# Kernel tuning notes

Hardware: AMD Instinct MI355X
Metric: run time of the kernel (lower is better)

The kernel has to match this reference:

```python
import jax, jax.numpy as jnp
import numpy as np
from jax import lax

LRELU_SLOPE = 0.2
EPS = 1e-8


def eq_linear(x, W, b):
    # EqualizedLinear: weight scaled by 1/sqrt(fan_in)
    c = 1.0 / np.sqrt(W.shape[1])
    return x @ (W * c).T + b


def mod_conv(x, s, W, demod):
    # x: [b, cin, h, w], s: [b, cin], W: [cout, cin, k, k]
    b, cin, h, w = x.shape
    cout, _, k, _ = W.shape
    c = 1.0 / np.sqrt(cin * k * k)
    weights = (W * c)[None] * s[:, None, :, None, None]  # [b, cout, cin, k, k]
    if demod:
        sigma_inv = lax.rsqrt(jnp.sum(weights ** 2, axis=(2, 3, 4)) + EPS)  # [b, cout]
        weights = weights * sigma_inv[:, :, None, None, None]
    x2 = x.reshape(1, b * cin, h, w)
    wk = weights.reshape(b * cout, cin, k, k)
    pad = k // 2
    out = lax.conv_general_dilated(
        x2, wk, window_strides=(1, 1), padding=[(pad, pad), (pad, pad)],
        dimension_numbers=("NCHW", "OIHW", "NCHW"), feature_group_count=b)
    return out.reshape(b, cout, h, w)


def style_block(x, w, noise, style_W, style_b, conv_W, scale_noise, bias):
    A = eq_linear(w, style_W, style_b)          # [b, cin]
    x = mod_conv(x, A, conv_W, demod=True)      # [b, cout, h, w]
    if noise is not None:
        x = x + scale_noise[None, :, None, None] * noise
    return jax.nn.leaky_relu(x + bias[None, :, None, None], LRELU_SLOPE)


def rgb_block(x, w, style_W, style_b, conv_W, bias):
    A = eq_linear(w, style_W, style_b)
    x = mod_conv(x, A, conv_W, demod=False)     # 1x1 conv to 3 channels
    return jax.nn.leaky_relu(x + bias[None, :, None, None], LRELU_SLOPE)


def setup_inputs() -> dict:
    key = jax.random.key(0)
    ks = jax.random.split(key, 10)
    B, CIN, COUT, WD, H, W = 8, 512, 512, 512, 64, 64
    return {
        "x": jax.random.normal(ks[0], (B, CIN, H, W), jnp.float32),
        "w": jax.random.normal(ks[1], (B, WD), jnp.float32),
        "noise": jax.random.normal(ks[2], (2, B, 1, H, W), jnp.float32),
        # StyleBlock 1
        "s1_style_W": jax.random.normal(ks[3], (CIN, WD), jnp.float32),
        "s1_style_b": jnp.ones((CIN,), jnp.float32),
        "s1_conv_W": jax.random.normal(ks[4], (COUT, CIN, 3, 3), jnp.float32),
        "s1_scale_noise": jnp.zeros((1,), jnp.float32),
        "s1_bias": jnp.zeros((COUT,), jnp.float32),
        # StyleBlock 2
        "s2_style_W": jax.random.normal(ks[5], (COUT, WD), jnp.float32),
        "s2_style_b": jnp.ones((COUT,), jnp.float32),
        "s2_conv_W": jax.random.normal(ks[6], (COUT, COUT, 3, 3), jnp.float32),
        "s2_scale_noise": jnp.zeros((1,), jnp.float32),
        "s2_bias": jnp.zeros((COUT,), jnp.float32),
        # RGBBlock
        "rgb_style_W": jax.random.normal(ks[7], (COUT, WD), jnp.float32),
        "rgb_style_b": jnp.ones((COUT,), jnp.float32),
        "rgb_conv_W": jax.random.normal(ks[8], (3, COUT, 1, 1), jnp.float32),
        "rgb_bias": jnp.zeros((3,), jnp.float32),
    }


def reference(x, w, noise,
              s1_style_W, s1_style_b, s1_conv_W, s1_scale_noise, s1_bias,
              s2_style_W, s2_style_b, s2_conv_W, s2_scale_noise, s2_bias,
              rgb_style_W, rgb_style_b, rgb_conv_W, rgb_bias):
    x = style_block(x, w, noise[0], s1_style_W, s1_style_b, s1_conv_W, s1_scale_noise, s1_bias)
    x = style_block(x, w, noise[1], s2_style_W, s2_style_b, s2_conv_W, s2_scale_noise, s2_bias)
    rgb = rgb_block(x, w, rgb_style_W, rgb_style_b, rgb_conv_W, rgb_bias)
    return (x, rgb)
```

## Files before the change

kernel.cpp:

```cpp
#include <hip/hip_runtime.h>
#include <stdint.h>

typedef __attribute__((ext_vector_type(8))) short bf16x8;
typedef __attribute__((ext_vector_type(4))) float f32x4;

__device__ __forceinline__ ushort f2bf(float f) {
  uint32_t u = __builtin_bit_cast(uint32_t, f);
  u += 0x7fffu + ((u >> 16) & 1u);
  return (ushort)(u >> 16);
}

__device__ __forceinline__ void async_copy16(const void* gsrc, void* ldst) {
  __builtin_amdgcn_global_load_lds(
      (const __attribute__((address_space(1))) void*)gsrc,
      (__attribute__((address_space(3))) void*)ldst, 16, 0, 0);
}

__global__ void style_linear3(const float* __restrict__ w,
                              const float* __restrict__ sW1, const float* __restrict__ sb1,
                              const float* __restrict__ sW2, const float* __restrict__ sb2,
                              const float* __restrict__ sW3, const float* __restrict__ sb3,
                              float* __restrict__ A1, float* __restrict__ A2,
                              float* __restrict__ A3) {
  const int which = blockIdx.z;
  const float* sW = (which == 0) ? sW1 : (which == 1) ? sW2 : sW3;
  const float* sb = (which == 0) ? sb1 : (which == 1) ? sb2 : sb3;
  float* A = (which == 0) ? A1 : (which == 1) ? A2 : A3;
  const int b = blockIdx.y;
  const int lane = threadIdx.x & 63, wv = threadIdx.x >> 6;
  const int co = blockIdx.x * 4 + wv;
  const float c = 0.04419417382415922f;
  const float* wr = w + b * 512;
  const float* Wr = sW + (size_t)co * 512;
  float s = 0.f;
#pragma unroll
  for (int i = 0; i < 8; ++i) {
    const int d = i * 64 + lane;
    s += wr[d] * Wr[d];
  }
#pragma unroll
  for (int off = 32; off; off >>= 1) s += __shfl_xor(s, off);
  if (lane == 0) A[b * 512 + co] = s * c + sb[co];
}

__global__ void prep_sigma(const float* __restrict__ Wc, const float* __restrict__ A,
                           ushort* __restrict__ Wt, float* __restrict__ sig) {
  const int co = blockIdx.x;
  const int ci = threadIdx.x;
  const int lane = ci & 63, wid = ci >> 6;
  const float c = 0.014731391274719738f;
  const float* src = Wc + ((size_t)co * 512 + ci) * 9;
  float s = 0.f;
#pragma unroll
  for (int t = 0; t < 9; ++t) {
    float v = src[t] * c;
    Wt[(size_t)t * 262144 + co * 512 + ci] = f2bf(v);
    s += v * v;
  }
  __shared__ float red[8][8];
#pragma unroll
  for (int b = 0; b < 8; ++b) {
    float a = A[b * 512 + ci];
    float v = s * a * a;
#pragma unroll
    for (int off = 32; off; off >>= 1) v += __shfl_xor(v, off);
    if (lane == 0) red[b][wid] = v;
  }
  __syncthreads();
  if (ci < 8) {
    float t = 0.f;
#pragma unroll
    for (int wv = 0; wv < 8; ++wv) t += red[ci][wv];
    sig[ci * 512 + co] = rsqrtf(t + 1e-8f);
  }
}

__global__ void zero_border(uint4* __restrict__ x1, uint4* __restrict__ x2,
                            uint4* __restrict__ rgb) {
  const int i = blockIdx.x * 256 + threadIdx.x;
  const int per = 16640;
  const int tot = per * 8;
  if (i >= 2 * tot) {
    const int j = i - 2 * tot;
    if (j < 24576) rgb[j] = make_uint4(0u, 0u, 0u, 0u);
    return;
  }
  uint4* base = (i < tot) ? x1 : x2;
  int t = (i < tot) ? i : i - tot;
  const int bb = t / per;
  int r = t - bb * per;
  int row, cell, q;
  if (r < 8448) {
    row = (r >= 4224) ? 65 : 0;
    int pos = (r >= 4224) ? r - 4224 : r;
    cell = pos >> 6;
    q = pos & 63;
  } else {
    int r2 = r - 8448;
    row = 1 + (r2 >> 7);
    cell = ((r2 >> 6) & 1) ? 65 : 0;
    q = r2 & 63;
  }
  base[(((size_t)bb * 66 + row) * 66 + cell) * 64 + q] = make_uint4(0u, 0u, 0u, 0u);
}

__global__ void mod_transpose(const float* __restrict__ X, const float* __restrict__ A,
                              ushort* __restrict__ xs) {
  __shared__ float tile[128][65];
  const int h = blockIdx.x;
  const int ci0 = blockIdx.y * 128;
  const int b = blockIdx.z;
  const int tid = threadIdx.x;
  const int wcol = tid & 63;
  const int r0 = tid >> 6;
#pragma unroll 4
  for (int i = 0; i < 32; ++i) {
    const int cil = r0 + i * 4;
    const int ci = ci0 + cil;
    const size_t off = ((size_t)(b * 512 + ci) * 64 + h) * 64 + wcol;
    tile[cil][wcol] = X[off] * A[b * 512 + ci];
  }
  __syncthreads();
  const int sub = tid & 3;
  const int w = tid >> 2;
  ushort* dst = xs + (((size_t)b * 66 + (h + 1)) * 66 + (w + 1)) * 512 + ci0 + sub * 32;
#pragma unroll
  for (int g = 0; g < 4; ++g) {
    bf16x8 v;
#pragma unroll
    for (int j = 0; j < 8; ++j) v[j] = (short)f2bf(tile[sub * 32 + g * 8 + j][w]);
    *(bf16x8*)(dst + g * 8) = v;
  }
}

#define WAITVM(N) __builtin_amdgcn_s_waitcnt(0x0F70 | (N))
#define SGB __builtin_amdgcn_sched_group_barrier

#define READS(S, AF, BV)                                                     \
  do {                                                                       \
    const int q_ = (S) & 3;                                                  \
    const char* baA = (const char*)(&smA[0][0] + q_ * 8192);                 \
    const char* baB = (const char*)(&smB[0][0] + q_ * 8192);                 \
    _Pragma("unroll") for (int m_ = 0; m_ < 8; ++m_)                         \
        AF[m_] = *(const bf16x8*)(baA + aro[m_]);                            \
    _Pragma("unroll") for (int n_ = 0; n_ < 4; ++n_)                         \
        BV[n_] = *(const bf16x8*)(baB + bro[n_]);                            \
  } while (0)

#define PH(S, WN, DOREAD, DOSTAGE, RAF, RBV, MAF, MBV)                               \
  do {                                                                               \
    WAITVM(WN);                                                                      \
    __builtin_amdgcn_s_barrier();                                                    \
    __builtin_amdgcn_sched_barrier(0);                                               \
    __builtin_amdgcn_s_setprio(1);                                                   \
    if (DOREAD) READS((S) + 1, RAF, RBV);                                            \
    if (DOSTAGE) stage((S) + 3);                                                     \
    _Pragma("unroll") for (int m_ = 0; m_ < 8; ++m_)                                 \
      _Pragma("unroll") for (int n_ = 0; n_ < 4; ++n_)                               \
        acc[m_][n_] = __builtin_amdgcn_mfma_f32_16x16x32_bf16(MAF[m_], MBV[n_],      \
                                                              acc[m_][n_], 0, 0, 0); \
    SGB(0x8, 2, 0);                                                                  \
    SGB(0x100, 2, 0); SGB(0x8, 4, 0);                                                \
    SGB(0x100, 2, 0); SGB(0x8, 4, 0);                                                \
    SGB(0x100, 2, 0); SGB(0x8, 4, 0);                                                \
    SGB(0x100, 2, 0); SGB(0x8, 4, 0);                                                \
    SGB(0x100, 2, 0); SGB(0x8, 4, 0);                                                \
    SGB(0x100, 2, 0); SGB(0x8, 6, 0);                                                \
    __builtin_amdgcn_s_setprio(0);                                                   \
    __builtin_amdgcn_sched_barrier(0);                                               \
  } while (0)

template <int OUT_MODE>
__global__ __launch_bounds__(512, 2) void conv3x3(
    const ushort* __restrict__ xs, const ushort* __restrict__ Wt,
    const float* __restrict__ sig, const float* __restrict__ noise,
    const float* __restrict__ scale_noise, const float* __restrict__ bias,
    const float* __restrict__ amod, void* __restrict__ outp,
    const float* __restrict__ rgbw, const float* __restrict__ arr,
    float* __restrict__ outrgb) {
  __shared__ __align__(16) ushort smA[4][8192];
  __shared__ __align__(16) ushort smB[4][8192];
  const int tid = threadIdx.x, lane = tid & 63, wid = tid >> 6;
  const int wr = wid >> 2, wc = wid & 3;
  const int id = blockIdx.x;
  const int b = id & 7;
  const int tile = id >> 3;
  const int co0 = (tile & 1) * 256;
  const int px0 = (tile >> 1) * 256;
  const int h0 = px0 >> 6;

  const int sswz = ((lane & 3) ^ ((lane >> 3) & 3)) * 8;
  int aoff[2], boff[2];
  ushort *ldsA[2], *ldsB[2];
#pragma unroll
  for (int i = 0; i < 2; ++i) {
    const int row = (i * 8 + wid) * 16 + (lane >> 2);
    aoff[i] = (co0 + row) * 512 + sswz;
    const int hh = h0 + (row >> 6), ww = row & 63;
    boff[i] = ((b * 66 + hh) * 66 + ww) * 512 + sswz;
    ldsA[i] = &smA[0][0] + (i * 8 + wid) * 512 + lane * 8;
    ldsB[i] = &smB[0][0] + (i * 8 + wid) * 512 + lane * 8;
  }
  const int rdsw = ((lane >> 4) ^ ((lane >> 1) & 3)) * 16;
  int aro[8], bro[4];
#pragma unroll
  for (int m = 0; m < 8; ++m) aro[m] = (wr * 128 + m * 16 + (lane & 15)) * 64 + rdsw;
#pragma unroll
  for (int n = 0; n < 4; ++n) bro[n] = (wc * 64 + n * 16 + (lane & 15)) * 64 + rdsw;

  f32x4 acc[8][4];
#pragma unroll
  for (int m = 0; m < 8; ++m)
#pragma unroll
    for (int n = 0; n < 4; ++n) acc[m][n] = (f32x4){0.f, 0.f, 0.f, 0.f};

  auto stage = [&](int s) {
    const int tap = s >> 4;
    const int ci0 = (s & 15) << 5;
    const int kh = tap / 3;
    const int kw = tap - kh * 3;
    const int q = s & 3;
    const ushort* Wb = Wt + tap * 262144 + ci0;
    const ushort* Xb = xs + (kh * 66 + kw) * 512 + ci0;
    async_copy16(Wb + aoff[0], ldsA[0] + q * 8192);
    async_copy16(Wb + aoff[1], ldsA[1] + q * 8192);
    async_copy16(Xb + boff[0], ldsB[0] + q * 8192);
    async_copy16(Xb + boff[1], ldsB[1] + q * 8192);
  };

  bf16x8 afA[8], bvA[4], afB[8], bvB[4];

  stage(0);
  stage(1);
  stage(2);
  WAITVM(8);
  __builtin_amdgcn_s_barrier();
  __builtin_amdgcn_sched_barrier(0);
  READS(0, afA, bvA);

  for (int s = 0; s < 140; s += 2) {
    PH(s, 4, true, true, afB, bvB, afA, bvA);
    PH(s + 1, 4, true, true, afA, bvA, afB, bvB);
  }
  PH(140, 4, true, true, afB, bvB, afA, bvA);
  PH(141, 4, true, false, afA, bvA, afB, bvB);
  PH(142, 0, true, false, afB, bvB, afA, bvA);
  PH(143, 0, false, false, afA, bvA, afB, bvB);

  const float sn = scale_noise[0];
  const int colp = lane & 15;
  const int rq = (lane >> 4) * 4;
  float nz[4];
#pragma unroll
  for (int n = 0; n < 4; ++n)
    nz[n] = sn * noise[b * 4096 + px0 + wc * 64 + n * 16 + colp];
  float rgbp[3][4];
#pragma unroll
  for (int c = 0; c < 3; ++c)
#pragma unroll
    for (int n = 0; n < 4; ++n) rgbp[c][n] = 0.f;
#pragma unroll
  for (int m = 0; m < 8; ++m) {
    const int cob = co0 + wr * 128 + m * 16 + rq;
    float sg[4], bs[4], am[4];
    float w0[4], w1[4], w2[4];
#pragma unroll
    for (int r = 0; r < 4; ++r) {
      sg[r] = sig[b * 512 + cob + r];
      bs[r] = bias[cob + r];
      if (OUT_MODE == 0) {
        am[r] = amod[b * 512 + cob + r];
      } else {
        const float a3 = arr[b * 512 + cob + r] * 0.04419417382415922f;
        w0[r] = rgbw[cob + r] * a3;
        w1[r] = rgbw[512 + cob + r] * a3;
        w2[r] = rgbw[1024 + cob + r] * a3;
      }
    }
#pragma unroll
    for (int n = 0; n < 4; ++n) {
      const int px = px0 + wc * 64 + n * 16 + colp;
      if (OUT_MODE == 0) {
        const int hh = px >> 6, ww = px & 63;
        ushort pk[4];
#pragma unroll
        for (int r = 0; r < 4; ++r) {
          float v = acc[m][n][r] * sg[r] + nz[n] + bs[r];
          v = (v > 0.f) ? v : 0.2f * v;
          pk[r] = f2bf(v * am[r]);
        }
        uint2 u;
        u.x = (uint32_t)pk[0] | ((uint32_t)pk[1] << 16);
        u.y = (uint32_t)pk[2] | ((uint32_t)pk[3] << 16);
        *(uint2*)((ushort*)outp + (((size_t)b * 66 + hh + 1) * 66 + (ww + 1)) * 512 + cob) = u;
      } else {
#pragma unroll
        for (int r = 0; r < 4; ++r) {
          float v = acc[m][n][r] * sg[r] + nz[n] + bs[r];
          v = (v > 0.f) ? v : 0.2f * v;
          ((float*)outp)[((size_t)b * 512 + cob + r) * 4096 + px] = v;
          rgbp[0][n] += w0[r] * v;
          rgbp[1][n] += w1[r] * v;
          rgbp[2][n] += w2[r] * v;
        }
      }
    }
  }
  if (OUT_MODE == 1) {
#pragma unroll
    for (int c = 0; c < 3; ++c)
#pragma unroll
      for (int n = 0; n < 4; ++n) {
        float s = rgbp[c][n];
        s += __shfl_xor(s, 16);
        s += __shfl_xor(s, 32);
        if (lane < 16)
          atomicAdd(&outrgb[((size_t)b * 3 + c) * 4096 + px0 + wc * 64 + n * 16 + colp], s);
      }
  }
}

__global__ void rgb_finish(float* __restrict__ o, const float* __restrict__ rb) {
  const int i = blockIdx.x * 256 + threadIdx.x;
  if (i >= 98304) return;
  const int c = (i >> 12) % 3;
  float v = o[i] + rb[c];
  o[i] = (v > 0.f) ? v : 0.2f * v;
}

extern "C" void kernel_launch(void* const* d_in, const int* in_sizes, int n_in,
                              void* d_out, int out_size, void* d_ws, size_t ws_size,
                              hipStream_t stream) {
  const float* x     = (const float*)d_in[0];
  const float* w     = (const float*)d_in[1];
  const float* noise = (const float*)d_in[2];
  const float* s1_sW = (const float*)d_in[3];
  const float* s1_sb = (const float*)d_in[4];
  const float* s1_cW = (const float*)d_in[5];
  const float* s1_sn = (const float*)d_in[6];
  const float* s1_b  = (const float*)d_in[7];
  const float* s2_sW = (const float*)d_in[8];
  const float* s2_sb = (const float*)d_in[9];
  const float* s2_cW = (const float*)d_in[10];
  const float* s2_sn = (const float*)d_in[11];
  const float* s2_b  = (const float*)d_in[12];
  const float* r_sW  = (const float*)d_in[13];
  const float* r_sb  = (const float*)d_in[14];
  const float* r_cW  = (const float*)d_in[15];
  const float* r_b   = (const float*)d_in[16];

  char* ws = (char*)d_ws;
  float*  A1  = (float*)(ws + 0);
  float*  A2  = (float*)(ws + 16384);
  float*  Arr = (float*)(ws + 32768);
  float*  sg1 = (float*)(ws + 49152);
  float*  sg2 = (float*)(ws + 65536);
  ushort* Wt1 = (ushort*)(ws + 98304);
  ushort* xs1 = (ushort*)(ws + 4816896);
  ushort* Wt2 = (ushort*)(ws + 4816896);
  ushort* xs2 = (ushort*)(ws + 40501248);
  float* outx   = (float*)d_out;
  float* outrgb = outx + (size_t)8 * 512 * 4096;

  style_linear3<<<dim3(128, 8, 3), 256, 0, stream>>>(w, s1_sW, s1_sb, s2_sW, s2_sb, r_sW,
                                                     r_sb, A1, A2, Arr);

  prep_sigma<<<512, 512, 0, stream>>>(s1_cW, A1, Wt1, sg1);

  zero_border<<<1136, 256, 0, stream>>>((uint4*)xs1, (uint4*)xs2, (uint4*)outrgb);
  mod_transpose<<<dim3(64, 4, 8), 256, 0, stream>>>(x, A1, xs1);

  conv3x3<0><<<dim3(256), 512, 0, stream>>>(xs1, Wt1, sg1, noise, s1_sn, s1_b, A2, (void*)xs2,
                                            r_cW, Arr, outrgb);
  prep_sigma<<<512, 512, 0, stream>>>(s2_cW, A2, Wt2, sg2);
  conv3x3<1><<<dim3(256), 512, 0, stream>>>(xs2, Wt2, sg2, noise + 32768, s2_sn, s2_b, sg2,
                                            (void*)outx, r_cW, Arr, outrgb);
  rgb_finish<<<384, 256, 0, stream>>>(outrgb, r_b);
}
```

Baseline: 314.0 us.

## Switch conv GEMM to 32x32x16 MFMA and drop sched-group interleaving

Replaces the 16x16x32 bf16 MFMA tiling with 32x32x16 MFMA instructions and remaps the LDS read offsets, accumulator layout and epilogue indexing to match the new fragment layout. The larger MFMA shape needs fewer instructions and fewer LDS fragment reads per unit of work. The explicit sched_group_barrier interleaving of LDS reads with MFMAs is removed and replaced by a hard barrier, so the reads for the next step now run before the MFMA block. That may reduce overlap between reads and math.

```diff
diff --git a/kernel.cpp b/kernel.cpp
--- a/kernel.cpp
+++ b/kernel.cpp
@@ -3,6 +3,7 @@
 
 typedef __attribute__((ext_vector_type(8))) short bf16x8;
 typedef __attribute__((ext_vector_type(4))) float f32x4;
+typedef __attribute__((ext_vector_type(16))) float f32x16;
 
 __device__ __forceinline__ ushort f2bf(float f) {
   uint32_t u = __builtin_bit_cast(uint32_t, f);
@@ -134,17 +135,16 @@
 }
 
 #define WAITVM(N) __builtin_amdgcn_s_waitcnt(0x0F70 | (N))
-#define SGB __builtin_amdgcn_sched_group_barrier
 
 #define READS(S, AF, BV)                                                     \
   do {                                                                       \
     const int q_ = (S) & 3;                                                  \
     const char* baA = (const char*)(&smA[0][0] + q_ * 8192);                 \
     const char* baB = (const char*)(&smB[0][0] + q_ * 8192);                 \
-    _Pragma("unroll") for (int m_ = 0; m_ < 8; ++m_)                         \
-        AF[m_] = *(const bf16x8*)(baA + aro[m_]);                            \
-    _Pragma("unroll") for (int n_ = 0; n_ < 4; ++n_)                         \
-        BV[n_] = *(const bf16x8*)(baB + bro[n_]);                            \
+    _Pragma("unroll") for (int r_ = 0; r_ < 8; ++r_)                         \
+        AF[r_] = *(const bf16x8*)(baA + aro[r_]);                            \
+    _Pragma("unroll") for (int r_ = 0; r_ < 4; ++r_)                         \
+        BV[r_] = *(const bf16x8*)(baB + bro[r_]);                            \
   } while (0)
 
 #define PH(S, WN, DOREAD, DOSTAGE, RAF, RBV, MAF, MBV)                               \
@@ -152,20 +152,15 @@
     WAITVM(WN);                                                                      \
     __builtin_amdgcn_s_barrier();                                                    \
     __builtin_amdgcn_sched_barrier(0);                                               \
-    __builtin_amdgcn_s_setprio(1);                                                   \
     if (DOREAD) READS((S) + 1, RAF, RBV);                                            \
     if (DOSTAGE) stage((S) + 3);                                                     \
-    _Pragma("unroll") for (int m_ = 0; m_ < 8; ++m_)                                 \
-      _Pragma("unroll") for (int n_ = 0; n_ < 4; ++n_)                               \
-        acc[m_][n_] = __builtin_amdgcn_mfma_f32_16x16x32_bf16(MAF[m_], MBV[n_],      \
-                                                              acc[m_][n_], 0, 0, 0); \
-    SGB(0x8, 2, 0);                                                                  \
-    SGB(0x100, 2, 0); SGB(0x8, 4, 0);                                                \
-    SGB(0x100, 2, 0); SGB(0x8, 4, 0);                                                \
-    SGB(0x100, 2, 0); SGB(0x8, 4, 0);                                                \
-    SGB(0x100, 2, 0); SGB(0x8, 4, 0);                                                \
-    SGB(0x100, 2, 0); SGB(0x8, 4, 0);                                                \
-    SGB(0x100, 2, 0); SGB(0x8, 6, 0);                                                \
+    __builtin_amdgcn_sched_barrier(0);                                               \
+    __builtin_amdgcn_s_setprio(1);                                                   \
+    _Pragma("unroll") for (int mi_ = 0; mi_ < 4; ++mi_)                              \
+      _Pragma("unroll") for (int ni_ = 0; ni_ < 2; ++ni_)                            \
+        _Pragma("unroll") for (int ks_ = 0; ks_ < 2; ++ks_)                          \
+          acc[mi_][ni_] = __builtin_amdgcn_mfma_f32_32x32x16_bf16(                   \
+              MAF[mi_ * 2 + ks_], MBV[ni_ * 2 + ks_], acc[mi_][ni_], 0, 0, 0);       \
     __builtin_amdgcn_s_setprio(0);                                                   \
     __builtin_amdgcn_sched_barrier(0);                                               \
   } while (0)
@@ -201,18 +196,27 @@
     ldsA[i] = &smA[0][0] + (i * 8 + wid) * 512 + lane * 8;
     ldsB[i] = &smB[0][0] + (i * 8 + wid) * 512 + lane * 8;
   }
-  const int rdsw = ((lane >> 4) ^ ((lane >> 1) & 3)) * 16;
   int aro[8], bro[4];
 #pragma unroll
-  for (int m = 0; m < 8; ++m) aro[m] = (wr * 128 + m * 16 + (lane & 15)) * 64 + rdsw;
-#pragma unroll
-  for (int n = 0; n < 4; ++n) bro[n] = (wc * 64 + n * 16 + (lane & 15)) * 64 + rdsw;
-
-  f32x4 acc[8][4];
-#pragma unroll
-  for (int m = 0; m < 8; ++m)
-#pragma unroll
-    for (int n = 0; n < 4; ++n) acc[m][n] = (f32x4){0.f, 0.f, 0.f, 0.f};
+  for (int mi = 0; mi < 4; ++mi)
+#pragma unroll
+    for (int ks = 0; ks < 2; ++ks)
+      aro[mi * 2 + ks] = (wr * 128 + mi * 32 + (lane & 31)) * 64 +
+                         (((ks * 2 + (lane >> 5)) ^ ((lane >> 1) & 3)) << 4);
+#pragma unroll
+  for (int ni = 0; ni < 2; ++ni)
+#pragma unroll
+    for (int ks = 0; ks < 2; ++ks)
+      bro[ni * 2 + ks] = (wc * 64 + ni * 32 + (lane & 31)) * 64 +
+                         (((ks * 2 + (lane >> 5)) ^ ((lane >> 1) & 3)) << 4);
+
+  f32x16 acc[4][2];
+#pragma unroll
+  for (int mi = 0; mi < 4; ++mi)
+#pragma unroll
+    for (int ni = 0; ni < 2; ++ni)
+#pragma unroll
+      for (int r = 0; r < 16; ++r) acc[mi][ni][r] = 0.f;
 
   auto stage = [&](int s) {
     const int tap = s >> 4;
@@ -248,60 +252,63 @@
   PH(143, 0, false, false, afA, bvA, afB, bvB);
 
   const float sn = scale_noise[0];
-  const int colp = lane & 15;
-  const int rq = (lane >> 4) * 4;
-  float nz[4];
-#pragma unroll
-  for (int n = 0; n < 4; ++n)
-    nz[n] = sn * noise[b * 4096 + px0 + wc * 64 + n * 16 + colp];
-  float rgbp[3][4];
+  const int pxl = lane & 31;
+  const int rh = (lane >> 5) * 4;
+  float nz[2];
+#pragma unroll
+  for (int ni = 0; ni < 2; ++ni)
+    nz[ni] = sn * noise[b * 4096 + px0 + wc * 64 + ni * 32 + pxl];
+  float rgbp[3][2];
 #pragma unroll
   for (int c = 0; c < 3; ++c)
 #pragma unroll
-    for (int n = 0; n < 4; ++n) rgbp[c][n] = 0.f;
-#pragma unroll
-  for (int m = 0; m < 8; ++m) {
-    const int cob = co0 + wr * 128 + m * 16 + rq;
-    float sg[4], bs[4], am[4];
-    float w0[4], w1[4], w2[4];
-#pragma unroll
-    for (int r = 0; r < 4; ++r) {
-      sg[r] = sig[b * 512 + cob + r];
-      bs[r] = bias[cob + r];
-      if (OUT_MODE == 0) {
-        am[r] = amod[b * 512 + cob + r];
-      } else {
-        const float a3 = arr[b * 512 + cob + r] * 0.04419417382415922f;
-        w0[r] = rgbw[cob + r] * a3;
-        w1[r] = rgbw[512 + cob + r] * a3;
-        w2[r] = rgbw[1024 + cob + r] * a3;
+    for (int ni = 0; ni < 2; ++ni) rgbp[c][ni] = 0.f;
+#pragma unroll
+  for (int mi = 0; mi < 4; ++mi) {
+#pragma unroll
+    for (int g = 0; g < 4; ++g) {
+      const int cob = co0 + wr * 128 + mi * 32 + g * 8 + rh;
+      float sg[4], bs[4], am[4];
+      float w0[4], w1[4], w2[4];
+#pragma unroll
+      for (int r = 0; r < 4; ++r) {
+        sg[r] = sig[b * 512 + cob + r];
+        bs[r] = bias[cob + r];
+        if (OUT_MODE == 0) {
+          am[r] = amod[b * 512 + cob + r];
+        } else {
+          const float a3 = arr[b * 512 + cob + r] * 0.04419417382415922f;
+          w0[r] = rgbw[cob + r] * a3;
+          w1[r] = rgbw[512 + cob + r] * a3;
+          w2[r] = rgbw[1024 + cob + r] * a3;
+        }
       }
-    }
-#pragma unroll
-    for (int n = 0; n < 4; ++n) {
-      const int px = px0 + wc * 64 + n * 16 + colp;
-      if (OUT_MODE == 0) {
-        const int hh = px >> 6, ww = px & 63;
-        ushort pk[4];
-#pragma unroll
-        for (int r = 0; r < 4; ++r) {
-          float v = acc[m][n][r] * sg[r] + nz[n] + bs[r];
-          v = (v > 0.f) ? v : 0.2f * v;
-          pk[r] = f2bf(v * am[r]);
-        }
-        uint2 u;
-        u.x = (uint32_t)pk[0] | ((uint32_t)pk[1] << 16);
-        u.y = (uint32_t)pk[2] | ((uint32_t)pk[3] << 16);
-        *(uint2*)((ushort*)outp + (((size_t)b * 66 + hh + 1) * 66 + (ww + 1)) * 512 + cob) = u;
-      } else {
-#pragma unroll
-        for (int r = 0; r < 4; ++r) {
-          float v = acc[m][n][r] * sg[r] + nz[n] + bs[r];
-          v = (v > 0.f) ? v : 0.2f * v;
-          ((float*)outp)[((size_t)b * 512 + cob + r) * 4096 + px] = v;
-          rgbp[0][n] += w0[r] * v;
-          rgbp[1][n] += w1[r] * v;
-          rgbp[2][n] += w2[r] * v;
+#pragma unroll
+      for (int ni = 0; ni < 2; ++ni) {
+        const int px = px0 + wc * 64 + ni * 32 + pxl;
+        if (OUT_MODE == 0) {
+          const int hh = px >> 6, ww = px & 63;
+          ushort pk[4];
+#pragma unroll
+          for (int r = 0; r < 4; ++r) {
+            float v = acc[mi][ni][g * 4 + r] * sg[r] + nz[ni] + bs[r];
+            v = (v > 0.f) ? v : 0.2f * v;
+            pk[r] = f2bf(v * am[r]);
+          }
+          uint2 u;
+          u.x = (uint32_t)pk[0] | ((uint32_t)pk[1] << 16);
+          u.y = (uint32_t)pk[2] | ((uint32_t)pk[3] << 16);
+          *(uint2*)((ushort*)outp + (((size_t)b * 66 + hh + 1) * 66 + (ww + 1)) * 512 + cob) = u;
+        } else {
+#pragma unroll
+          for (int r = 0; r < 4; ++r) {
+            float v = acc[mi][ni][g * 4 + r] * sg[r] + nz[ni] + bs[r];
+            v = (v > 0.f) ? v : 0.2f * v;
+            ((float*)outp)[((size_t)b * 512 + cob + r) * 4096 + px] = v;
+            rgbp[0][ni] += w0[r] * v;
+            rgbp[1][ni] += w1[r] * v;
+            rgbp[2][ni] += w2[r] * v;
+          }
         }
       }
     }
@@ -310,12 +317,11 @@
 #pragma unroll
     for (int c = 0; c < 3; ++c)
 #pragma unroll
-      for (int n = 0; n < 4; ++n) {
-        float s = rgbp[c][n];
-        s += __shfl_xor(s, 16);
+      for (int ni = 0; ni < 2; ++ni) {
+        float s = rgbp[c][ni];
         s += __shfl_xor(s, 32);
-        if (lane < 16)
-          atomicAdd(&outrgb[((size_t)b * 3 + c) * 4096 + px0 + wc * 64 + n * 16 + colp], s);
+        if (lane < 32)
+          atomicAdd(&outrgb[((size_t)b * 3 + c) * 4096 + px0 + wc * 64 + ni * 32 + lane], s);
       }
   }
 }
```

Result: slower. 428.1 us (+36.4%).
